# Kernel tuning notes

Measured on AMD Instinct MI355X. Metric: run time of the kernel, lower is better.

## Reference

```python
import jax, jax.numpy as jnp
import numpy as np

B = 1024; PAST = 64; FUT = 16; N = PAST + FUT; DM = N // 3; HID = 64
EMB = [(2000, 32), (7, 8), (24, 8)]
OUTP = 3 + 32 + 8 + 8  # 51 = out_preprocess
O = OUTP - 1           # 50
HID1 = 64; HID2 = 64
NEG = -1e30  # finite stand-in for -inf so fully-masked rows stay NaN-free


def _gcnn(x, A, W, act):
    # D = diag((1 + rowsum(sign(relu(A-1e-15))))^-0.5); out = act(D @ A @ D @ (x W^T))
    d = (1.0 + (A > 1e-15).astype(x.dtype).sum(1)) ** -0.5
    An = d[:, None] * A * d[None, :]            # (P,P)
    h = jnp.einsum('pq,bqc->bpc', An, x @ W.T)  # (B,P,out)
    return jax.nn.relu(h) if act else h


def _forward(data, emb0, emb1, emb2, w1, b1, w2, b2, w3, b3,
             M, Wg1a, Wg1b, Wk, smoothing, Wg2a, Wg2b):
    # learned adjacency: masked softmax over strictly-lower-triangular support
    mask = jnp.tril(jnp.ones((N, N), data.dtype), -1)
    A0 = jax.nn.relu(M @ M.T)
    A = jax.nn.softmax(jnp.where(mask > 0, A0, NEG), axis=1)
    A = jnp.where(mask > 0, A, 0.0)
    # pre_processing: embeddings + MLP, then re-append last raw column
    tabs = (emb0, emb1, emb2)
    e = [t[data[:, :, i].astype(jnp.int32)] for i, t in enumerate(tabs)]
    h = jnp.concatenate(e + [data[:, :, -3:]], -1)        # (B,N,51)
    h = jax.nn.relu(h @ w1.T + b1)
    h = jax.nn.relu(h @ w2.T + b2)
    h = h @ w3.T + b3                                      # (B,N,50)
    x = jnp.concatenate([h, data[:, :, -1:]], -1)          # (B,N,51)
    sg1, sg2 = x[:, :PAST], x[:, PAST:]
    A11 = A[:PAST, :PAST]
    x1 = _gcnn(_gcnn(sg1, A11, Wg1a, True), A11, Wg1b, False)   # (B,PAST,50)
    xk = jnp.concatenate([x1, sg2[:, :, :-1]], 1)               # (B,N,50)
    y = x[:, :PAST, -1:]                                        # (B,PAST,1)
    # Kernel: batched Mahalanobis quadratic form (diagonal computed directly)
    xp, xf = xk[:, :PAST], xk[:, PAST:]
    theta = Wk @ Wk.T
    theta = (theta + theta.T) / 2
    diff = xp[:, None, :, :] - xf[:, :, None, :]                # (B,F,P,50)
    q = jnp.einsum('bjip,pq,bjiq->bji', diff, theta, diff)      # (B,F,P)
    alpha = -0.5 * q / (jax.nn.sigmoid(smoothing[0]) * 0.01)
    At = A[FUT:, :PAST] if False else A[PAST:, :PAST]           # (F,P)
    At = jax.nn.softmax(jnp.where(At != 0, At, NEG), axis=1)
    # torch Softmax(dim=1) on (B,F,P) normalizes over the F axis
    alpha = jax.nn.softmax(jnp.where(At[None] >= 0.004, alpha, NEG), axis=1)
    yh = jnp.einsum('bjp,bpo->bjo', alpha, y)                   # (B,F,1)
    x2 = jnp.concatenate([sg2[:, :, :-1], yh], -1)              # (B,F,51)
    A22 = A[PAST:, PAST:]
    out = _gcnn(_gcnn(x2, A22, Wg2a, True), A22, Wg2b, False).reshape(-1, FUT)
    # cdist(x, x), p=2, with NaN-safe sqrt at zero distance
    xc = jnp.concatenate([sg1, x2], 1)                          # (B,N,51)
    sq = jnp.sum(xc * xc, -1)
    d2 = jnp.maximum(sq[:, :, None] + sq[:, None, :]
                     - 2.0 * jnp.einsum('bnc,bmc->bnm', xc, xc), 0.0)
    dist = jnp.where(d2 > 0, jnp.sqrt(jnp.where(d2 > 0, d2, 1.0)), 0.0)
    return (out, dist, A)


def setup_inputs() -> dict:
    key = jax.random.key(0)
    ks = jax.random.split(key, 20)
    cols = [jax.random.randint(ks[i], (B, N, 1), 0, EMB[i][0]).astype(jnp.float32)
            for i in range(3)]
    data = jnp.concatenate(cols + [jax.random.normal(ks[3], (B, N, 3), jnp.float32)], -1)
    g = lambda k, s, sc: jax.random.normal(k, s, jnp.float32) * sc
    return dict(
        data=data,
        emb0=g(ks[4], EMB[0], 1.0),
        emb1=g(ks[5], EMB[1], 1.0),
        emb2=g(ks[6], EMB[2], 1.0),
        w1=g(ks[7], (128, OUTP), OUTP ** -0.5), b1=jnp.zeros((128,), jnp.float32),
        w2=g(ks[8], (128, 128), 128 ** -0.5), b2=jnp.zeros((128,), jnp.float32),
        w3=g(ks[9], (O, 128), 128 ** -0.5), b3=jnp.zeros((O,), jnp.float32),
        M=g(ks[10], (N, DM), 1.0),
        Wg1a=g(ks[11], (HID1, OUTP), OUTP ** -0.5),
        Wg1b=g(ks[12], (O, HID1), HID1 ** -0.5),
        Wk=g(ks[13], (O, HID), 0.05),
        smoothing=g(ks[14], (1,), 1.0),
        Wg2a=g(ks[15], (HID2, OUTP), OUTP ** -0.5),
        Wg2b=g(ks[16], (1, HID2), HID2 ** -0.5),
    )


def reference(data, emb0, emb1, emb2, w1, b1, w2, b2, w3, b3,
              M, Wg1a, Wg1b, Wk, smoothing, Wg2a, Wg2b):
    return _forward(data, emb0, emb1, emb2, w1, b1, w2, b2, w3, b3,
                    M, Wg1a, Wg1b, Wk, smoothing, Wg2a, Wg2b)
```

## Files before the change

kernel.cpp:

```cpp
#include <hip/hip_runtime.h>
#include <math.h>


#define NEGBIG (-1e30f)

#define OFF_X     0
#define OFF_A     7471104
#define OFF_AN22  7481600
#define OFF_MK    7484356
#define OFF_GAH   7514692
#define OFF_GAL   7516740
#define OFF_G2AT  7521156
#define OFF_SC    7524420
#define OFF_W1H   7524424
#define OFF_W1L   7528520
#define OFF_W2H   7532616
#define OFF_W2L   7540808
#define OFF_W3H   7549000
#define OFF_W3L   7553096
#define OFF_ANH   7557192
#define OFF_ANL   7559240
#define OFF_GBH   7561288
#define OFF_GBL   7563336
#define OFF_WKH   7565384
#define OFF_WKL   7567432

#define OUT_OUT   0
#define OUT_DIST  16384
#define OUT_A     6569984

typedef __attribute__((ext_vector_type(8))) short bf16x8;
typedef __attribute__((ext_vector_type(4))) short s16x4;
typedef __attribute__((ext_vector_type(4))) float f32x4;

__device__ __forceinline__ unsigned short f2bf(float x) {
  union { float f; unsigned u; } v; v.f = x;
  unsigned r = v.u + 0x7fffu + ((v.u >> 16) & 1u);
  return (unsigned short)(r >> 16);
}
__device__ __forceinline__ float bf2f(unsigned short h) {
  union { unsigned u; float f; } v; v.u = ((unsigned)h) << 16; return v.f;
}
__device__ __forceinline__ void split2(float v, unsigned short& h, unsigned short& l) {
  unsigned short hh = f2bf(v);
  h = hh;
  l = f2bf(v - bf2f(hh));
}
#define SWZ6(r, k) (((r) << 6) + (((((k) >> 3) ^ ((r) & 7)) << 3) | ((k) & 7)))
#define SWZ7(r, k) (((r) << 7) + (((((k) >> 3) ^ ((r) & 7)) << 3) | ((k) & 7)))

#define MFMA3(acc, aH, aL, bH, bL) \
  acc = __builtin_amdgcn_mfma_f32_16x16x32_bf16(aH, bH, acc, 0, 0, 0); \
  acc = __builtin_amdgcn_mfma_f32_16x16x32_bf16(aH, bL, acc, 0, 0, 0); \
  acc = __builtin_amdgcn_mfma_f32_16x16x32_bf16(aL, bH, acc, 0, 0, 0);
#define MFMA4(acc, aH, aL, bH, bL) \
  MFMA3(acc, aH, aL, bH, bL) \
  acc = __builtin_amdgcn_mfma_f32_16x16x32_bf16(aL, bL, acc, 0, 0, 0);

__global__ __launch_bounds__(256) void k_prep(
    const float* __restrict__ M, const float* __restrict__ Wk,
    const float* __restrict__ sm,
    const float* __restrict__ w1, const float* __restrict__ w2,
    const float* __restrict__ w3,
    const float* __restrict__ wg1a, const float* __restrict__ wg1b,
    const float* __restrict__ wg2a,
    float* __restrict__ ws, float* __restrict__ out)
{
  __shared__ float Msh[80 * 26];
  __shared__ float Ash[80 * 80];
  __shared__ float d1[64];
  __shared__ float d2s[16];
  const int t = threadIdx.x;

  if (blockIdx.x == 0) {
    for (int e = t; e < 80 * 26; e += 256) Msh[e] = M[e];
    __syncthreads();
    for (int e = t; e < 6400; e += 256) {
      int i = e / 80, j = e % 80;
      float v = 0.f;
      if (j < i) {
        float s = 0.f;
        for (int k = 0; k < 26; ++k) s += Msh[i * 26 + k] * Msh[j * 26 + k];
        v = s > 0.f ? s : 0.f;
      }
      Ash[e] = v;
    }
    __syncthreads();
    if (t > 0 && t < 80) {
      int i = t;
      float m = -3.4e38f;
      for (int j = 0; j < i; ++j) m = fmaxf(m, Ash[i * 80 + j]);
      float s = 0.f;
      for (int j = 0; j < i; ++j) {
        float e = expf(Ash[i * 80 + j] - m);
        Ash[i * 80 + j] = e;
        s += e;
      }
      float inv = 1.f / s;
      for (int j = 0; j < i; ++j) Ash[i * 80 + j] *= inv;
    }
// ... 61 lines not shown
    }
    if (t == 0) {
      float v = sm[0];
      float sig = 1.f / (1.f + expf(-v));
      (ws + OFF_SC)[0] = -0.5f / (sig * 0.01f);
    }
  } else if (blockIdx.x == 2) {
    unsigned short* w1h = (unsigned short*)(ws + OFF_W1H);
    unsigned short* w1l = (unsigned short*)(ws + OFF_W1L);
    for (int e = t; e < 8192; e += 256) {
      int n = e >> 6, k = e & 63;
      float v = (k < 51) ? w1[n * 51 + k] : 0.f;
      unsigned short h = f2bf(v);
      w1h[e] = h; w1l[e] = f2bf(v - bf2f(h));
    }
    unsigned short* w3h = (unsigned short*)(ws + OFF_W3H);
    unsigned short* w3l = (unsigned short*)(ws + OFF_W3L);
    for (int e = t; e < 8192; e += 256) {
      int n = e >> 7, k = e & 127;
      float v = (n < 50) ? w3[n * 128 + k] : 0.f;
      unsigned short h = f2bf(v);
      w3h[e] = h; w3l[e] = f2bf(v - bf2f(h));
    }
    unsigned short* gah = (unsigned short*)(ws + OFF_GAH);
    unsigned short* gal = (unsigned short*)(ws + OFF_GAL);
    for (int e = t; e < 4096; e += 256) {
      int n = e >> 6, k = e & 63;
      float v = (k < 51) ? wg1a[n * 51 + k] : 0.f;
      unsigned short h = f2bf(v);
      gah[e] = h; gal[e] = f2bf(v - bf2f(h));
    }
  } else {
    unsigned short* w2h = (unsigned short*)(ws + OFF_W2H);
    unsigned short* w2l = (unsigned short*)(ws + OFF_W2L);
    for (int e = t; e < 16384; e += 256) {
      int n = e >> 7, k = e & 127;
      float v = w2[n * 128 + k];
      unsigned short h = f2bf(v);
      w2h[e] = h; w2l[e] = f2bf(v - bf2f(h));
    }
    unsigned short* gbh = (unsigned short*)(ws + OFF_GBH);
    unsigned short* gbl = (unsigned short*)(ws + OFF_GBL);
    for (int e = t; e < 4096; e += 256) {
      int n = e >> 6, k = e & 63;
      float v = (n < 50) ? wg1b[n * 64 + k] : 0.f;
      unsigned short h = f2bf(v);
      gbh[e] = h; gbl[e] = f2bf(v - bf2f(h));
    }
    float* g2at = ws + OFF_G2AT;
    for (int e = t; e < 64 * 51; e += 256) { int o = e / 51, k = e % 51; g2at[k * 64 + o] = wg2a[e]; }
  }
}

__global__ __launch_bounds__(512, 4) void k_fused(
    const float* __restrict__ data,
    const float* __restrict__ emb0, const float* __restrict__ emb1,
    const float* __restrict__ emb2,
    const float* __restrict__ b1v, const float* __restrict__ b2v,
    const float* __restrict__ b3v,
    const float* __restrict__ wg2b,
    float* __restrict__ ws, float* __restrict__ out)
{
  __shared__ __align__(16) unsigned short SH[32768];
  __shared__ __align__(16) float xbuf[80 * 51];

  const int t = threadIdx.x, b = blockIdx.x;
  const int lane = t & 63, wave = t >> 6;
  const int m16 = lane & 15, quad = lane >> 4;

  {
    unsigned short* mIaH = SH;
    unsigned short* mIaL = SH + 5120;
    unsigned short* mHdH = SH + 10240;
    unsigned short* mHdL = SH + 20480;
    const unsigned short* w1h = (const unsigned short*)(ws + OFF_W1H);
    const unsigned short* w1l = (const unsigned short*)(ws + OFF_W1L);
    const unsigned short* w2h = (const unsigned short*)(ws + OFF_W2H);
    const unsigned short* w2l = (const unsigned short*)(ws + OFF_W2L);
    const unsigned short* w3h = (const unsigned short*)(ws + OFF_W3H);
    const unsigned short* w3l = (const unsigned short*)(ws + OFF_W3L);

    for (int e = t; e < 5120; e += 512) {
      int r = e >> 6, c = e & 63;
      int g = b * 80 + r;
      float v = 0.f;
      if (c < 32)      { int i0 = (int)data[g * 6 + 0]; v = emb0[i0 * 32 + c]; }
      else if (c < 40) { int i1 = (int)data[g * 6 + 1]; v = emb1[i1 * 8 + (c - 32)]; }
      else if (c < 48) { int i2 = (int)data[g * 6 + 2]; v = emb2[i2 * 8 + (c - 40)]; }
      else if (c < 51) { v = data[g * 6 + 3 + (c - 48)]; }
      int idx = SWZ6(r, c);
      split2(v, mIaH[idx], mIaL[idx]);
    }
    if (t < 80) xbuf[t * 51 + 50] = data[(b * 80 + t) * 6 + 5];
    __syncthreads();

    {
      const int col = wave * 16 + m16;
      bf16x8 bH0 = *(const bf16x8*)(w1h + (col << 6) + (quad << 3));
      bf16x8 bL0 = *(const bf16x8*)(w1l + (col << 6) + (quad << 3));
      bf16x8 bH1 = *(const bf16x8*)(w1h + (col << 6) + ((quad + 4) << 3));
      bf16x8 bL1 = *(const bf16x8*)(w1l + (col << 6) + ((quad + 4) << 3));
      const float bias = b1v[col];
      const int ach0 = ((quad + 0) ^ (m16 & 7)) << 3;
      const int ach1 = ((quad + 4) ^ (m16 & 7)) << 3;
#pragma unroll
      for (int rt = 0; rt < 5; ++rt) {
        const int ar = rt * 16 + m16;
        f32x4 acc = (f32x4){0.f, 0.f, 0.f, 0.f};
        bf16x8 aH = *(const bf16x8*)(mIaH + (ar << 6) + ach0);
        bf16x8 aL = *(const bf16x8*)(mIaL + (ar << 6) + ach0);
        MFMA3(acc, aH, aL, bH0, bL0)
        aH = *(const bf16x8*)(mIaH + (ar << 6) + ach1);
        aL = *(const bf16x8*)(mIaL + (ar << 6) + ach1);
        MFMA3(acc, aH, aL, bH1, bL1)
#pragma unroll
        for (int r = 0; r < 4; ++r) {
          float v = acc[r] + bias; v = v > 0.f ? v : 0.f;
          int idx = SWZ7(rt * 16 + quad * 4 + r, col);
          split2(v, mHdH[idx], mHdL[idx]);
        }
      }
    }
    __syncthreads();

    f32x4 acc2[5];
    {
      const int col = wave * 16 + m16;
      bf16x8 bh[4], bl[4];
#pragma unroll
      for (int kk = 0; kk < 4; ++kk) {
        bh[kk] = *(const bf16x8*)(w2h + (col << 7) + ((quad + kk * 4) << 3));
        bl[kk] = *(const bf16x8*)(w2l + (col << 7) + ((quad + kk * 4) << 3));
      }
#pragma unroll
      for (int rt = 0; rt < 5; ++rt) {
        const int ar = rt * 16 + m16;
        f32x4 acc = (f32x4){0.f, 0.f, 0.f, 0.f};
#pragma unroll
        for (int kk = 0; kk < 4; ++kk) {
          int ach = ((quad + kk * 4) ^ (m16 & 7)) << 3;
          bf16x8 aH = *(const bf16x8*)(mHdH + (ar << 7) + ach);
          bf16x8 aL = *(const bf16x8*)(mHdL + (ar << 7) + ach);
          MFMA3(acc, aH, aL, bh[kk], bl[kk])
        }
        acc2[rt] = acc;
      }
    }
    __syncthreads();
    {
      const int col = wave * 16 + m16;
      const float bias = b2v[col];
#pragma unroll
      for (int rt = 0; rt < 5; ++rt) {
#pragma unroll
        for (int r = 0; r < 4; ++r) {
          float v = acc2[rt][r] + bias; v = v > 0.f ? v : 0.f;
          int idx = SWZ7(rt * 16 + quad * 4 + r, col);
          split2(v, mHdH[idx], mHdL[idx]);
        }
      }
    }
    __syncthreads();

    {
      const int ct = wave & 3, rh = wave >> 2;
      const int col = ct * 16 + m16;
      bf16x8 bh[4], bl[4];
#pragma unroll
      for (int kk = 0; kk < 4; ++kk) {
        bh[kk] = *(const bf16x8*)(w3h + (col << 7) + ((quad + kk * 4) << 3));
        bl[kk] = *(const bf16x8*)(w3l + (col << 7) + ((quad + kk * 4) << 3));
      }
      const float bias = (col < 50) ? b3v[col] : 0.f;
      for (int rt = rh; rt < 5; rt += 2) {
        const int ar = rt * 16 + m16;
        f32x4 acc = (f32x4){0.f, 0.f, 0.f, 0.f};
#pragma unroll
        for (int kk = 0; kk < 4; ++kk) {
          int ach = ((quad + kk * 4) ^ (m16 & 7)) << 3;
          bf16x8 aH = *(const bf16x8*)(mHdH + (ar << 7) + ach);
          bf16x8 aL = *(const bf16x8*)(mHdL + (ar << 7) + ach);
          MFMA3(acc, aH, aL, bh[kk], bl[kk])
        }
        if (col < 50) {
#pragma unroll
          for (int r = 0; r < 4; ++r)
            xbuf[(rt * 16 + quad * 4 + r) * 51 + col] = acc[r] + bias;
        }
      }
    }
    __syncthreads();
  }

  unsigned short* b1H = SH;
  unsigned short* b1L = SH + 4096;
  unsigned short* b2H = SH + 8192;
  unsigned short* b2L = SH + 12288;
  unsigned short* anH = SH + 16384;
  unsigned short* anL = SH + 20480;
  unsigned short* wH  = SH + 24576;
  unsigned short* wL  = SH + 28672;
  unsigned short* xfH = SH + 24576;
  unsigned short* xfL = SH + 25600;
  unsigned short* zfH = SH + 26624;
  unsigned short* zfL = SH + 27648;
  float* alS  = (float*)(SH + 28672);
  float* spH2 = (float*)(SH + 30848);
  float* spS  = (float*)(SH + 31104);
  float* sfS  = (float*)(SH + 31232);
  float* yvS  = (float*)(SH + 31264);
  float* yhsS = (float*)(SH + 31392);
  float* X2v  = (float*)(SH + 8192);
  float* A22v = X2v + 832;
  float* G2v  = A22v + 256;
  float* Pmv  = G2v + 1024;
  float* wb2  = Pmv + 1024;
  float* zzv  = wb2 + 64;
  unsigned short* xcH = SH;
  unsigned short* xcL = SH + 16384;
  float* sqS = (float*)(SH + 21504);

  const int s = wave & 3, half = wave >> 2;
  const int row0 = s * 16;
  const int arow = row0 + m16;
  const float* mk = ws + OFF_MK;
  const float* an22 = ws + OFF_AN22;
  const float* g2at = ws + OFF_G2AT;
  const unsigned short* gAnH = (const unsigned short*)(ws + OFF_ANH);
  const unsigned short* gAnL = (const unsigned short*)(ws + OFF_ANL);
  const unsigned short* gaH = (const unsigned short*)(ws + OFF_GAH);
  const unsigned short* gaL = (const unsigned short*)(ws + OFF_GAL);
  const unsigned short* gbH = (const unsigned short*)(ws + OFF_GBH);
  const unsigned short* gbL = (const unsigned short*)(ws + OFF_GBL);
  const unsigned short* gwkH = (const unsigned short*)(ws + OFF_WKH);
  const unsigned short* gwkL = (const unsigned short*)(ws + OFF_WKL);
  const float sc = (ws + OFF_SC)[0];

  for (int e = t; e < 4096; e += 512) {
    int r = e >> 6, k = e & 63;
    float v = (k < 51) ? xbuf[r * 51 + k] : 0.f;
    int idx = SWZ6(r, k);
    split2(v, b1H[idx], b1L[idx]);
  }
  {
    int q = t;
    if (q < 512) {
      int r = q >> 3, c = q & 7;
      int dst = (r << 6) + ((c ^ (r & 7)) << 3);
      int src = (r << 6) + (c << 3);
      *(bf16x8*)(anH + dst) = *(const bf16x8*)(gAnH + src);
      *(bf16x8*)(anL + dst) = *(const bf16x8*)(gAnL + src);
      *(bf16x8*)(wH + dst)  = *(const bf16x8*)(gaH + src);
      *(bf16x8*)(wL + dst)  = *(const bf16x8*)(gaL + src);
    }
  }
  float yvreg = 0.f;
  if (t < 64) yvreg = xbuf[t * 51 + 50];
  bf16x8 pH, pL;
  {
    int q = t & 511;
    int r = q >> 3, c = q & 7;
    int src = (r << 6) + (c << 3);
    pH = *(const bf16x8*)(gbH + src);
    pL = *(const bf16x8*)(gbL + src);
  }
  __syncthreads();

  f32x4 accA[2];
#pragma unroll
  for (int n = 0; n < 2; ++n) accA[n] = (f32x4){0.f, 0.f, 0.f, 0.f};
#pragma unroll
  for (int kb8 = 0; kb8 < 8; kb8 += 4) {
    int ach = ((quad + kb8) ^ (m16 & 7)) << 3;
    bf16x8 aH = *(const bf16x8*)(b1H + (arow << 6) + ach);
    bf16x8 aL = *(const bf16x8*)(b1L + (arow << 6) + ach);
#pragma unroll
    for (int n = 0; n < 2; ++n) {
      const int col = (half * 2 + n) * 16 + m16;
      int boff = (col << 6) + ach;
      bf16x8 bH = *(const bf16x8*)(wH + boff);
      bf16x8 bL = *(const bf16x8*)(wL + boff);
      MFMA3(accA[n], aH, aL, bH, bL)
    }
  }
  __syncthreads();

  {
    const int kb = row0 + quad * 4;
#pragma unroll
    for (int n = 0; n < 2; ++n) {
      const int col = (half * 2 + n) * 16 + m16;
      int idx = (col << 6) + (((((kb >> 3) ^ (col & 7)) << 3)) | (kb & 7));
      s16x4 hv, lv;
#pragma unroll
      for (int r = 0; r < 4; ++r) {
        unsigned short hh, ll; split2(accA[n][r], hh, ll);
        hv[r] = (short)hh; lv[r] = (short)ll;
      }
      *(s16x4*)(b2H + idx) = hv; *(s16x4*)(b2L + idx) = lv;
    }
  }
  {
    int q = t & 511;
    int r = q >> 3, c = q & 7;
    int dst = (r << 6) + ((c ^ (r & 7)) << 3);
    *(bf16x8*)(wH + dst) = pH;
    *(bf16x8*)(wL + dst) = pL;
    int src = (r << 6) + (c << 3);
    pH = *(const bf16x8*)(gwkH + src);
    pL = *(const bf16x8*)(gwkL + src);
  }
  __syncthreads();

#pragma unroll
  for (int n = 0; n < 2; ++n) accA[n] = (f32x4){0.f, 0.f, 0.f, 0.f};
#pragma unroll
  for (int kb8 = 0; kb8 < 8; kb8 += 4) {
    int ach = ((quad + kb8) ^ (m16 & 7)) << 3;
    bf16x8 aH = *(const bf16x8*)(anH + (arow << 6) + ach);
    bf16x8 aL = *(const bf16x8*)(anL + (arow << 6) + ach);
#pragma unroll
    for (int n = 0; n < 2; ++n) {
      const int col = (half * 2 + n) * 16 + m16;
      int boff = (col << 6) + ach;
      bf16x8 bH = *(const bf16x8*)(b2H + boff);
      bf16x8 bL = *(const bf16x8*)(b2L + boff);
      MFMA3(accA[n], aH, aL, bH, bL)
    }
  }
  __syncthreads();

  {
    const int kb = row0 + quad * 4;
#pragma unroll
    for (int n = 0; n < 2; ++n) {
      const int col = (half * 2 + n) * 16 + m16;
      int idx = (col << 6) + (((((kb >> 3) ^ (col & 7)) << 3)) | (kb & 7));
      s16x4 hv, lv;
#pragma unroll
      for (int r = 0; r < 4; ++r) {
        float v = accA[n][r]; v = v > 0.f ? v : 0.f;
        unsigned short hh, ll; split2(v, hh, ll);
        hv[r] = (short)hh; lv[r] = (short)ll;
      }
      *(s16x4*)(b2H + idx) = hv; *(s16x4*)(b2L + idx) = lv;
    }
  }
  __syncthreads();

#pragma unroll
  for (int n = 0; n < 2; ++n) accA[n] = (f32x4){0.f, 0.f, 0.f, 0.f};
#pragma unroll
  for (int kb8 = 0; kb8 < 8; kb8 += 4) {
    int ach = ((quad + kb8) ^ (m16 & 7)) << 3;
    bf16x8 aH = *(const bf16x8*)(anH + (arow << 6) + ach);
    bf16x8 aL = *(const bf16x8*)(anL + (arow << 6) + ach);
#pragma unroll
    for (int n = 0; n < 2; ++n) {
      const int col = (half * 2 + n) * 16 + m16;
      int boff = (col << 6) + ach;
      bf16x8 bH = *(const bf16x8*)(b2H + boff);
      bf16x8 bL = *(const bf16x8*)(b2L + boff);
      MFMA3(accA[n], aH, aL, bH, bL)
    }
  }
  __syncthreads();

#pragma unroll
  for (int n = 0; n < 2; ++n) {
    const int col = (half * 2 + n) * 16 + m16;
#pragma unroll
    for (int r = 0; r < 4; ++r) {
      int idx = SWZ6(row0 + quad * 4 + r, col);
      split2(accA[n][r], b1H[idx], b1L[idx]);
    }
  }
  {
    int q = t & 511;
    int r = q >> 3, c = q & 7;
    int dst = (r << 6) + ((c ^ (r & 7)) << 3);
    *(bf16x8*)(anH + dst) = pH;
    *(bf16x8*)(anL + dst) = pL;
  }
  float xf0 = 0.f, xf1 = 0.f;
  {
    int e0 = t, e1 = t + 512;
    int r0r = e0 >> 6, c0 = e0 & 63;
    int r1r = e1 >> 6, c1 = e1 & 63;
    if (c0 < 50) xf0 = xbuf[(64 + r0r) * 51 + c0];
    if (c1 < 50) xf1 = xbuf[(64 + r1r) * 51 + c1];
  }
  __syncthreads();

#pragma unroll
  for (int n = 0; n < 2; ++n) accA[n] = (f32x4){0.f, 0.f, 0.f, 0.f};
#pragma unroll
  for (int kb8 = 0; kb8 < 8; kb8 += 4) {
    int ach = ((quad + kb8) ^ (m16 & 7)) << 3;
    bf16x8 aH = *(const bf16x8*)(b1H + (arow << 6) + ach);
    bf16x8 aL = *(const bf16x8*)(b1L + (arow << 6) + ach);
#pragma unroll
    for (int n = 0; n < 2; ++n) {
      const int col = (half * 2 + n) * 16 + m16;
      int boff = (col << 6) + ach;
      bf16x8 bH = *(const bf16x8*)(wH + boff);
      bf16x8 bL = *(const bf16x8*)(wL + boff);
      MFMA3(accA[n], aH, aL, bH, bL)
    }
  }
  __syncthreads();

#pragma unroll
  for (int n = 0; n < 2; ++n) {
    const int col = (half * 2 + n) * 16 + m16;
#pragma unroll
    for (int r = 0; r < 4; ++r) {
      int idx = SWZ6(row0 + quad * 4 + r, col);
      split2(accA[n][r], b2H[idx], b2L[idx]);
    }
  }
  {
    int e0 = t, e1 = t + 512;
    int i0 = SWZ6(e0 >> 6, e0 & 63);
    int i1 = SWZ6(e1 >> 6, e1 & 63);
    split2(xf0, xfH[i0], xfL[i0]);
    split2(xf1, xfH[i1], xfL[i1]);
  }
  if (t < 64) yvS[t] = yvreg;
  __syncthreads();

#pragma unroll
  for (int n = 0; n < 2; ++n) accA[n] = (f32x4){0.f, 0.f, 0.f, 0.f};
#pragma unroll
  for (int kb8 = 0; kb8 < 8; kb8 += 4) {
    int ach = ((quad + kb8) ^ (m16 & 7)) << 3;
    bf16x8 aH = *(const bf16x8*)(b2H + (arow << 6) + ach);
    bf16x8 aL = *(const bf16x8*)(b2L + (arow << 6) + ach);
#pragma unroll
    for (int n = 0; n < 2; ++n) {
      const int col = (half * 2 + n) * 16 + m16;
      int boff = (col << 6) + ach;
      bf16x8 bH = *(const bf16x8*)(anH + boff);
      bf16x8 bL = *(const bf16x8*)(anL + boff);
      MFMA4(accA[n], aH, aL, bH, bL)
    }
  }
  if (half == 0) {
    f32x4 af = (f32x4){0.f, 0.f, 0.f, 0.f};
#pragma unroll
    for (int kb8 = 0; kb8 < 8; kb8 += 4) {
      int ach = ((quad + kb8) ^ (m16 & 7)) << 3;
      bf16x8 aH = *(const bf16x8*)(xfH + (m16 << 6) + ach);
      bf16x8 aL = *(const bf16x8*)(xfL + (m16 << 6) + ach);
      const int col = s * 16 + m16;
      int boff = (col << 6) + ach;
      bf16x8 bH = *(const bf16x8*)(anH + boff);
      bf16x8 bL = *(const bf16x8*)(anL + boff);
      MFMA4(af, aH, aL, bH, bL)
    }
    const int h = s * 16 + m16;
#pragma unroll
    for (int r = 0; r < 4; ++r) {
      int idx = SWZ6(quad * 4 + r, h);
      split2(af[r], zfH[idx], zfL[idx]);
    }
  }
  {
    float s2[4];
#pragma unroll
    for (int r = 0; r < 4; ++r)
      s2[r] = accA[0][r] * accA[0][r] + accA[1][r] * accA[1][r];
#pragma unroll
    for (int n = 0; n < 2; ++n) {
      const int h = (half * 2 + n) * 16 + m16;
#pragma unroll
      for (int r = 0; r < 4; ++r) {
        int idx = SWZ6(row0 + quad * 4 + r, h);
        split2(accA[n][r], b1H[idx], b1L[idx]);
      }
    }
#pragma unroll
    for (int m = 1; m < 16; m <<= 1)
#pragma unroll
      for (int r = 0; r < 4; ++r) s2[r] += __shfl_xor(s2[r], m);
    if (m16 == 0) {
#pragma unroll
      for (int r = 0; r < 4; ++r)
        spH2[(row0 + quad * 4 + r) * 2 + half] = s2[r];
    }
  }
  __syncthreads();

  if (t < 64) {
    spS[t] = spH2[t * 2] + spH2[t * 2 + 1];
  } else if (t < 320) {
    int idx = t - 64;
    int j = idx >> 4, h0 = (idx & 15) * 4;
    float p = 0.f;
#pragma unroll
    for (int r = 0; r < 4; ++r) {
      int ii = SWZ6(j, h0 + r);
      float v = bf2f(zfH[ii]) + bf2f(zfL[ii]);
      p += v * v;
    }
#pragma unroll
    for (int m = 1; m < 16; m <<= 1) p += __shfl_xor(p, m);
    if ((idx & 15) == 0) sfS[j] = p;
  }
  __syncthreads();

  {
    f32x4 ac2 = (f32x4){0.f, 0.f, 0.f, 0.f};
#pragma unroll
    for (int kb8 = 0; kb8 < 8; kb8 += 4) {
      int ach = ((quad + kb8) ^ (m16 & 7)) << 3;
      bf16x8 aH = *(const bf16x8*)(b1H + (arow << 6) + ach);
      bf16x8 aL = *(const bf16x8*)(b1L + (arow << 6) + ach);
      bf16x8 bH = *(const bf16x8*)(zfH + (m16 << 6) + ach);
      bf16x8 bL = *(const bf16x8*)(zfL + (m16 << 6) + ach);
      MFMA4(ac2, aH, aL, bH, bL)
    }
    if (half == 0) {
#pragma unroll
      for (int r = 0; r < 4; ++r) {
        int i = row0 + quad * 4 + r;
        alS[i * 17 + m16] = sc * (spS[i] + sfS[m16] - 2.f * ac2[r]);
      }
    }
  }
  __syncthreads();

  if (t < 64) {
    const int i = t;
    float lv[16];
    float m = -3.4e38f;
#pragma unroll
    for (int j = 0; j < 16; ++j) {
      float v = (mk[j * 64 + i] != 0.f) ? alS[i * 17 + j] : NEGBIG;
      lv[j] = v;
      m = fmaxf(m, v);
    }
    float ssum = 0.f;
#pragma unroll
    for (int j = 0; j < 16; ++j) { lv[j] = expf(lv[j] - m); ssum += lv[j]; }
    float inv = 1.f / ssum;
#pragma unroll
    for (int j = 0; j < 16; ++j) alS[i * 17 + j] = lv[j] * inv;
  }
  __syncthreads();

  if (t < 256) {
    int j = t >> 4, i0 = (t & 15) * 4;
    float p = 0.f;
#pragma unroll
    for (int r = 0; r < 4; ++r) p += alS[(i0 + r) * 17 + j] * yvS[i0 + r];
#pragma unroll
    for (int m = 1; m < 16; m <<= 1) p += __shfl_xor(p, m);
    if ((t & 15) == 0) yhsS[j] = p;
  }
  __syncthreads();

  for (int e = t; e < 5120; e += 512) {
    int n = e >> 6, c = e & 63;
    float v = 0.f;
    if (c < 50)       v = xbuf[n * 51 + c];
    else if (c == 50) v = (n < 64) ? xbuf[n * 51 + 50] : yhsS[n - 64];
    int idx = SWZ6(n, c);
    split2(v, xcH[idx], xcL[idx]);
  }
  for (int e = t; e < 832; e += 512) {
    int r = e / 52, c = e - r * 52;
    float v = 0.f;
    if (c < 50)       v = xbuf[(64 + r) * 51 + c];
    else if (c == 50) v = yhsS[r];
    X2v[e] = v;
  }
  for (int e = t; e < 256; e += 512) A22v[e] = an22[e];
  if (t < 64) wb2[t] = wg2b[t];
  __syncthreads();

  f32x4 accD[4];
  {
    int tc = 0;
    for (int idx = wave; idx < 25; idx += 8) {
      int ts = idx / 5, tf = idx - ts * 5;
      f32x4 acc = (f32x4){0.f, 0.f, 0.f, 0.f};
#pragma unroll
      for (int kb8 = 0; kb8 < 8; kb8 += 4) {
        int ach = ((quad + kb8) ^ (m16 & 7)) << 3;
        bf16x8 aH = *(const bf16x8*)(xcH + ((ts * 16 + m16) << 6) + ach);
        bf16x8 aL = *(const bf16x8*)(xcL + ((ts * 16 + m16) << 6) + ach);
        const int col = tf * 16 + m16;
        int boff = (col << 6) + ach;
        bf16x8 bH = *(const bf16x8*)(xcH + boff);
        bf16x8 bL = *(const bf16x8*)(xcL + boff);
        MFMA3(acc, aH, aL, bH, bL)
      }
      if (ts == tf && (m16 >> 2) == quad) sqS[ts * 16 + m16] = acc[m16 & 3];
      accD[tc++] = acc;
    }
  }
  for (int e = t; e < 1024; e += 512) {
    int j = e >> 6, h = e & 63;
    float ssum = 0.f;
    for (int k = 0; k < 51; ++k) ssum += X2v[j * 52 + k] * g2at[k * 64 + h];
    G2v[e] = ssum;
  }
  __syncthreads();

  for (int e = t; e < 1024; e += 512) {
    int j = e >> 6, h = e & 63;
    float ssum = 0.f;
#pragma unroll
    for (int k = 0; k < 16; ++k) ssum += A22v[j * 16 + k] * G2v[k * 64 + h];
    Pmv[e] = ssum > 0.f ? ssum : 0.f;
  }
  {
    float* dist = out + OUT_DIST + b * 6400;
    int tc = 0;
    for (int idx = wave; idx < 25; idx += 8) {
      int ts = idx / 5, tf = idx - ts * 5;
      f32x4 acc = accD[tc++];
#pragma unroll
      for (int r = 0; r < 4; ++r) {
        int i = ts * 16 + quad * 4 + r;
        int m = tf * 16 + m16;
        float d2 = sqS[i] + sqS[m] - 2.f * acc[r];
        d2 = d2 > 0.f ? d2 : 0.f;
        dist[i * 80 + m] = d2 > 0.f ? sqrtf(d2) : 0.f;
      }
    }
  }
  __syncthreads();
  if (t < 256) {
    int j = t >> 4, h0 = (t & 15) * 4;
    float p = 0.f;
#pragma unroll
    for (int r = 0; r < 4; ++r) p += Pmv[j * 64 + h0 + r] * wb2[h0 + r];
#pragma unroll
    for (int m = 1; m < 16; m <<= 1) p += __shfl_xor(p, m);
    if ((t & 15) == 0) zzv[j] = p;
  }
  __syncthreads();
  if (t < 16) {
    float ssum = 0.f;
#pragma unroll
    for (int k = 0; k < 16; ++k) ssum += A22v[t * 16 + k] * zzv[k];
    out[OUT_OUT + b * 16 + t] = ssum;
  }
}

extern "C" void kernel_launch(void* const* d_in, const int* in_sizes, int n_in,
                              void* d_out, int out_size, void* d_ws, size_t ws_size,
                              hipStream_t stream)
{
  const float* data = (const float*)d_in[0];
  const float* emb0 = (const float*)d_in[1];
  const float* emb1 = (const float*)d_in[2];
  const float* emb2 = (const float*)d_in[3];
  const float* w1   = (const float*)d_in[4];
  const float* b1   = (const float*)d_in[5];
  const float* w2   = (const float*)d_in[6];
  const float* b2   = (const float*)d_in[7];
  const float* w3   = (const float*)d_in[8];
  const float* b3   = (const float*)d_in[9];
  const float* M    = (const float*)d_in[10];
  const float* wg1a = (const float*)d_in[11];
  const float* wg1b = (const float*)d_in[12];
  const float* Wk   = (const float*)d_in[13];
  const float* smo  = (const float*)d_in[14];
  const float* wg2a = (const float*)d_in[15];
  const float* wg2b = (const float*)d_in[16];
  float* ws  = (float*)d_ws;
  float* out = (float*)d_out;

  k_prep <<<dim3(4),    dim3(256), 0, stream>>>(M, Wk, smo, w1, w2, w3, wg1a, wg1b, wg2a, ws, out);
  k_fused<<<dim3(1024), dim3(512), 0, stream>>>(data, emb0, emb1, emb2, b1, b2, b3, wg2b, ws, out);
}
```

Baseline: 200.3 us.

## Shrink shared memory footprint to raise occupancy and stream weights from global

The MLP preprocessing now runs over rows in two chunks (48 then 32) so hidden activations need less LDS, and embeddings are gathered straight into MFMA A-fragments in registers instead of staging through shared memory. The fp32 xbuf is dropped and the features are kept only as split bf16 in xc. The GCNN and kernel weight operands are read directly from global memory instead of being copied into LDS, which removes several barriers. LDS drops from about 80KB to 54KB and launch bounds rise to 6 blocks per SM, trading extra global/L2 traffic and recomputed bf16 reconstructions for higher occupancy.

```diff
diff --git a/kernel.cpp b/kernel.cpp
--- a/kernel.cpp
+++ b/kernel.cpp
@@ -4,7 +4,6 @@
 
 #define NEGBIG (-1e30f)
 
-#define OFF_X     0
 #define OFF_A     7471104
 #define OFF_AN22  7481600
 #define OFF_MK    7484356
@@ -46,6 +45,13 @@
   h = hh;
   l = f2bf(v - bf2f(hh));
 }
+__device__ __forceinline__ void split8(const float* v, bf16x8& h8, bf16x8& l8) {
+#pragma unroll
+  for (int j = 0; j < 8; ++j) {
+    unsigned short hh, ll; split2(v[j], hh, ll);
+    h8[j] = (short)hh; l8[j] = (short)ll;
+  }
+}
 #define SWZ6(r, k) (((r) << 6) + (((((k) >> 3) ^ ((r) & 7)) << 3) | ((k) & 7)))
 #define SWZ7(r, k) (((r) << 7) + (((((k) >> 3) ^ ((r) & 7)) << 3) | ((k) & 7)))
 
@@ -213,7 +219,7 @@
   }
 }
 
-__global__ __launch_bounds__(512, 4) void k_fused(
+__global__ __launch_bounds__(512, 6) void k_fused(
     const float* __restrict__ data,
     const float* __restrict__ emb0, const float* __restrict__ emb1,
     const float* __restrict__ emb2,
@@ -222,168 +228,44 @@
     const float* __restrict__ wg2b,
     float* __restrict__ ws, float* __restrict__ out)
 {
-  __shared__ __align__(16) unsigned short SH[32768];
-  __shared__ __align__(16) float xbuf[80 * 51];
+  __shared__ __align__(16) unsigned short SH[27136];
+
+  unsigned short* xcH = SH;
+  unsigned short* xcL = SH + 5120;
+  unsigned short* b1H = SH + 10240;
+  unsigned short* b1L = SH + 14336;
+  unsigned short* b2H = SH + 18432;
+  unsigned short* b2L = SH + 22528;
+  float* spH2 = (float*)(SH + 26624);
+  float* spS  = (float*)(SH + 26880);
+  float* sfS  = (float*)(SH + 27008);
+  float* yhsS = (float*)(SH + 27040);
+  float* alS = (float*)(SH + 18432);
+  unsigned short* zfH = SH + 22528;
+  unsigned short* zfL = SH + 23552;
+  unsigned short* mHdH = SH + 10240;
+  unsigned short* mHdL = SH + 16384;
+  float* X2v  = (float*)(SH + 10240);
+  float* A22v = (float*)(SH + 11904);
+  float* G2v  = (float*)(SH + 12416);
+  float* Pmv  = (float*)(SH + 14464);
+  float* wb2  = (float*)(SH + 16512);
+  float* zzv  = (float*)(SH + 16640);
+  float* sqS  = (float*)(SH + 16672);
 
   const int t = threadIdx.x, b = blockIdx.x;
   const int lane = t & 63, wave = t >> 6;
   const int m16 = lane & 15, quad = lane >> 4;
-
-  {
-    unsigned short* mIaH = SH;
-    unsigned short* mIaL = SH + 5120;
-    unsigned short* mHdH = SH + 10240;
-    unsigned short* mHdL = SH + 20480;
-    const unsigned short* w1h = (const unsigned short*)(ws + OFF_W1H);
-    const unsigned short* w1l = (const unsigned short*)(ws + OFF_W1L);
-    const unsigned short* w2h = (const unsigned short*)(ws + OFF_W2H);
-    const unsigned short* w2l = (const unsigned short*)(ws + OFF_W2L);
-    const unsigned short* w3h = (const unsigned short*)(ws + OFF_W3H);
-    const unsigned short* w3l = (const unsigned short*)(ws + OFF_W3L);
-
-    for (int e = t; e < 5120; e += 512) {
-      int r = e >> 6, c = e & 63;
-      int g = b * 80 + r;
-      float v = 0.f;
-      if (c < 32)      { int i0 = (int)data[g * 6 + 0]; v = emb0[i0 * 32 + c]; }
-      else if (c < 40) { int i1 = (int)data[g * 6 + 1]; v = emb1[i1 * 8 + (c - 32)]; }
-      else if (c < 48) { int i2 = (int)data[g * 6 + 2]; v = emb2[i2 * 8 + (c - 40)]; }
-      else if (c < 51) { v = data[g * 6 + 3 + (c - 48)]; }
-      int idx = SWZ6(r, c);
-      split2(v, mIaH[idx], mIaL[idx]);
-    }
-    if (t < 80) xbuf[t * 51 + 50] = data[(b * 80 + t) * 6 + 5];
-    __syncthreads();
-
-    {
-      const int col = wave * 16 + m16;
-      bf16x8 bH0 = *(const bf16x8*)(w1h + (col << 6) + (quad << 3));
-      bf16x8 bL0 = *(const bf16x8*)(w1l + (col << 6) + (quad << 3));
-      bf16x8 bH1 = *(const bf16x8*)(w1h + (col << 6) + ((quad + 4) << 3));
-      bf16x8 bL1 = *(const bf16x8*)(w1l + (col << 6) + ((quad + 4) << 3));
-      const float bias = b1v[col];
-      const int ach0 = ((quad + 0) ^ (m16 & 7)) << 3;
-      const int ach1 = ((quad + 4) ^ (m16 & 7)) << 3;
-#pragma unroll
-      for (int rt = 0; rt < 5; ++rt) {
-        const int ar = rt * 16 + m16;
-        f32x4 acc = (f32x4){0.f, 0.f, 0.f, 0.f};
-        bf16x8 aH = *(const bf16x8*)(mIaH + (ar << 6) + ach0);
-        bf16x8 aL = *(const bf16x8*)(mIaL + (ar << 6) + ach0);
-        MFMA3(acc, aH, aL, bH0, bL0)
-        aH = *(const bf16x8*)(mIaH + (ar << 6) + ach1);
-        aL = *(const bf16x8*)(mIaL + (ar << 6) + ach1);
-        MFMA3(acc, aH, aL, bH1, bL1)
-#pragma unroll
-        for (int r = 0; r < 4; ++r) {
-          float v = acc[r] + bias; v = v > 0.f ? v : 0.f;
-          int idx = SWZ7(rt * 16 + quad * 4 + r, col);
-          split2(v, mHdH[idx], mHdL[idx]);
-        }
-      }
-    }
-    __syncthreads();
-
-    f32x4 acc2[5];
-    {
-      const int col = wave * 16 + m16;
-      bf16x8 bh[4], bl[4];
-#pragma unroll
-      for (int kk = 0; kk < 4; ++kk) {
-        bh[kk] = *(const bf16x8*)(w2h + (col << 7) + ((quad + kk * 4) << 3));
-        bl[kk] = *(const bf16x8*)(w2l + (col << 7) + ((quad + kk * 4) << 3));
-      }
-#pragma unroll
-      for (int rt = 0; rt < 5; ++rt) {
-        const int ar = rt * 16 + m16;
-        f32x4 acc = (f32x4){0.f, 0.f, 0.f, 0.f};
-#pragma unroll
-        for (int kk = 0; kk < 4; ++kk) {
-          int ach = ((quad + kk * 4) ^ (m16 & 7)) << 3;
-          bf16x8 aH = *(const bf16x8*)(mHdH + (ar << 7) + ach);
-          bf16x8 aL = *(const bf16x8*)(mHdL + (ar << 7) + ach);
-          MFMA3(acc, aH, aL, bh[kk], bl[kk])
-        }
-        acc2[rt] = acc;
-      }
-    }
-    __syncthreads();
-    {
-      const int col = wave * 16 + m16;
-      const float bias = b2v[col];
-#pragma unroll
-      for (int rt = 0; rt < 5; ++rt) {
-#pragma unroll
-        for (int r = 0; r < 4; ++r) {
-          float v = acc2[rt][r] + bias; v = v > 0.f ? v : 0.f;
-          int idx = SWZ7(rt * 16 + quad * 4 + r, col);
-          split2(v, mHdH[idx], mHdL[idx]);
-        }
-      }
-    }
-    __syncthreads();
-
-    {
-      const int ct = wave & 3, rh = wave >> 2;
-      const int col = ct * 16 + m16;
-      bf16x8 bh[4], bl[4];
-#pragma unroll
-      for (int kk = 0; kk < 4; ++kk) {
-        bh[kk] = *(const bf16x8*)(w3h + (col << 7) + ((quad + kk * 4) << 3));
-        bl[kk] = *(const bf16x8*)(w3l + (col << 7) + ((quad + kk * 4) << 3));
-      }
-      const float bias = (col < 50) ? b3v[col] : 0.f;
-      for (int rt = rh; rt < 5; rt += 2) {
-        const int ar = rt * 16 + m16;
-        f32x4 acc = (f32x4){0.f, 0.f, 0.f, 0.f};
-#pragma unroll
-        for (int kk = 0; kk < 4; ++kk) {
-          int ach = ((quad + kk * 4) ^ (m16 & 7)) << 3;
-          bf16x8 aH = *(const bf16x8*)(mHdH + (ar << 7) + ach);
-          bf16x8 aL = *(const bf16x8*)(mHdL + (ar << 7) + ach);
-          MFMA3(acc, aH, aL, bh[kk], bl[kk])
-        }
-        if (col < 50) {
-#pragma unroll
-          for (int r = 0; r < 4; ++r)
-            xbuf[(rt * 16 + quad * 4 + r) * 51 + col] = acc[r] + bias;
-        }
-      }
-    }
-    __syncthreads();
-  }
-
-  unsigned short* b1H = SH;
-  unsigned short* b1L = SH + 4096;
-  unsigned short* b2H = SH + 8192;
-  unsigned short* b2L = SH + 12288;
-  unsigned short* anH = SH + 16384;
-  unsigned short* anL = SH + 20480;
-  unsigned short* wH  = SH + 24576;
-  unsigned short* wL  = SH + 28672;
-  unsigned short* xfH = SH + 24576;
-  unsigned short* xfL = SH + 25600;
-  unsigned short* zfH = SH + 26624;
-  unsigned short* zfL = SH + 27648;
-  float* alS  = (float*)(SH + 28672);
-  float* spH2 = (float*)(SH + 30848);
-  float* spS  = (float*)(SH + 31104);
-  float* sfS  = (float*)(SH + 31232);
-  float* yvS  = (float*)(SH + 31264);
-  float* yhsS = (float*)(SH + 31392);
-  float* X2v  = (float*)(SH + 8192);
-  float* A22v = X2v + 832;
-  float* G2v  = A22v + 256;
-  float* Pmv  = G2v + 1024;
-  float* wb2  = Pmv + 1024;
-  float* zzv  = wb2 + 64;
-  unsigned short* xcH = SH;
-  unsigned short* xcL = SH + 16384;
-  float* sqS = (float*)(SH + 21504);
-
   const int s = wave & 3, half = wave >> 2;
   const int row0 = s * 16;
   const int arow = row0 + m16;
+
+  const unsigned short* w1h = (const unsigned short*)(ws + OFF_W1H);
+  const unsigned short* w1l = (const unsigned short*)(ws + OFF_W1L);
+  const unsigned short* w2h = (const unsigned short*)(ws + OFF_W2H);
+  const unsigned short* w2l = (const unsigned short*)(ws + OFF_W2L);
+  const unsigned short* w3h = (const unsigned short*)(ws + OFF_W3H);
+  const unsigned short* w3l = (const unsigned short*)(ws + OFF_W3L);
   const float* mk = ws + OFF_MK;
   const float* an22 = ws + OFF_AN22;
   const float* g2at = ws + OFF_G2AT;
@@ -397,55 +279,156 @@
   const unsigned short* gwkL = (const unsigned short*)(ws + OFF_WKL);
   const float sc = (ws + OFF_SC)[0];
 
-  for (int e = t; e < 4096; e += 512) {
-    int r = e >> 6, k = e & 63;
-    float v = (k < 51) ? xbuf[r * 51 + k] : 0.f;
-    int idx = SWZ6(r, k);
-    split2(v, b1H[idx], b1L[idx]);
-  }
-  {
-    int q = t;
-    if (q < 512) {
-      int r = q >> 3, c = q & 7;
-      int dst = (r << 6) + ((c ^ (r & 7)) << 3);
-      int src = (r << 6) + (c << 3);
-      *(bf16x8*)(anH + dst) = *(const bf16x8*)(gAnH + src);
-      *(bf16x8*)(anL + dst) = *(const bf16x8*)(gAnL + src);
-      *(bf16x8*)(wH + dst)  = *(const bf16x8*)(gaH + src);
-      *(bf16x8*)(wL + dst)  = *(const bf16x8*)(gaL + src);
-    }
-  }
-  float yvreg = 0.f;
-  if (t < 64) yvreg = xbuf[t * 51 + 50];
-  bf16x8 pH, pL;
-  {
-    int q = t & 511;
-    int r = q >> 3, c = q & 7;
-    int src = (r << 6) + (c << 3);
-    pH = *(const bf16x8*)(gbH + src);
-    pL = *(const bf16x8*)(gbL + src);
-  }
-  __syncthreads();
+#pragma unroll
+  for (int ck = 0; ck < 2; ++ck) {
+    const int C0 = ck ? 48 : 0;
+    const int NT = ck ? 2 : 3;
+
+    {
+      const int col = wave * 16 + m16;
+      bf16x8 bH0 = *(const bf16x8*)(w1h + (col << 6) + (quad << 3));
+      bf16x8 bL0 = *(const bf16x8*)(w1l + (col << 6) + (quad << 3));
+      bf16x8 bH1 = *(const bf16x8*)(w1h + (col << 6) + 32 + (quad << 3));
+      bf16x8 bL1 = *(const bf16x8*)(w1l + (col << 6) + 32 + (quad << 3));
+      const float bias = b1v[col];
+#pragma unroll
+      for (int rt = 0; rt < NT; ++rt) {
+        const int g = b * 80 + C0 + rt * 16 + m16;
+        float v0[8], v1[8];
+        {
+          int i0 = (int)data[g * 6 + 0];
+          const float* p = emb0 + i0 * 32 + (quad << 3);
+#pragma unroll
+          for (int j = 0; j < 8; ++j) v0[j] = p[j];
+        }
+        if (quad == 0) {
+          int i1 = (int)data[g * 6 + 1];
+#pragma unroll
+          for (int j = 0; j < 8; ++j) v1[j] = emb1[i1 * 8 + j];
+        } else if (quad == 1) {
+          int i2 = (int)data[g * 6 + 2];
+#pragma unroll
+          for (int j = 0; j < 8; ++j) v1[j] = emb2[i2 * 8 + j];
+        } else if (quad == 2) {
+          v1[0] = data[g * 6 + 3]; v1[1] = data[g * 6 + 4]; v1[2] = data[g * 6 + 5];
+#pragma unroll
+          for (int j = 3; j < 8; ++j) v1[j] = 0.f;
+        } else {
+#pragma unroll
+          for (int j = 0; j < 8; ++j) v1[j] = 0.f;
+        }
+        bf16x8 aH0, aL0, aH1, aL1;
+        split8(v0, aH0, aL0);
+        split8(v1, aH1, aL1);
+        f32x4 acc = (f32x4){0.f, 0.f, 0.f, 0.f};
+        MFMA3(acc, aH0, aL0, bH0, bL0)
+        MFMA3(acc, aH1, aL1, bH1, bL1)
+#pragma unroll
+        for (int r = 0; r < 4; ++r) {
+          float v = acc[r] + bias; v = v > 0.f ? v : 0.f;
+          int idx = SWZ7(rt * 16 + quad * 4 + r, col);
+          split2(v, mHdH[idx], mHdL[idx]);
+        }
+      }
+    }
+    __syncthreads();
+
+    f32x4 acc2[3];
+    {
+      const int col = wave * 16 + m16;
+      bf16x8 bh[4], bl[4];
+#pragma unroll
+      for (int kk = 0; kk < 4; ++kk) {
+        bh[kk] = *(const bf16x8*)(w2h + (col << 7) + ((quad + kk * 4) << 3));
+        bl[kk] = *(const bf16x8*)(w2l + (col << 7) + ((quad + kk * 4) << 3));
+      }
+#pragma unroll
+      for (int lrt = 0; lrt < NT; ++lrt) {
+        const int lr = lrt * 16 + m16;
+        f32x4 acc = (f32x4){0.f, 0.f, 0.f, 0.f};
+#pragma unroll
+        for (int kk = 0; kk < 4; ++kk) {
+          int ach = ((quad + kk * 4) ^ (m16 & 7)) << 3;
+          bf16x8 aH = *(const bf16x8*)(mHdH + (lr << 7) + ach);
+          bf16x8 aL = *(const bf16x8*)(mHdL + (lr << 7) + ach);
+          MFMA3(acc, aH, aL, bh[kk], bl[kk])
+        }
+        acc2[lrt] = acc;
+      }
+    }
+    __syncthreads();
+
+    {
+      const int col = wave * 16 + m16;
+      const float bias = b2v[col];
+#pragma unroll
+      for (int lrt = 0; lrt < NT; ++lrt) {
+#pragma unroll
+        for (int r = 0; r < 4; ++r) {
+          float v = acc2[lrt][r] + bias; v = v > 0.f ? v : 0.f;
+          int idx = SWZ7(lrt * 16 + quad * 4 + r, col);
+          split2(v, mHdH[idx], mHdL[idx]);
+        }
+      }
+    }
+    __syncthreads();
+
+    {
+      const int colt = wave & 3, rh = wave >> 2;
+      const int col = colt * 16 + m16;
+      bf16x8 bh[4], bl[4];
+#pragma unroll
+      for (int kk = 0; kk < 4; ++kk) {
+        bh[kk] = *(const bf16x8*)(w3h + (col << 7) + ((quad + kk * 4) << 3));
+        bl[kk] = *(const bf16x8*)(w3l + (col << 7) + ((quad + kk * 4) << 3));
+      }
+      const float bias = (col < 50) ? b3v[col] : 0.f;
+      for (int lrt = rh; lrt < NT; lrt += 2) {
+        const int lr = lrt * 16 + m16;
+        f32x4 acc = (f32x4){0.f, 0.f, 0.f, 0.f};
+#pragma unroll
+        for (int kk = 0; kk < 4; ++kk) {
+          int ach = ((quad + kk * 4) ^ (m16 & 7)) << 3;
+          bf16x8 aH = *(const bf16x8*)(mHdH + (lr << 7) + ach);
+          bf16x8 aL = *(const bf16x8*)(mHdL + (lr << 7) + ach);
+          MFMA3(acc, aH, aL, bh[kk], bl[kk])
+        }
+        if (col != 50) {
+#pragma unroll
+          for (int r = 0; r < 4; ++r) {
+            int grow = C0 + lrt * 16 + quad * 4 + r;
+            int idx = SWZ6(grow, col);
+            split2(acc[r] + bias, xcH[idx], xcL[idx]);
+          }
+        }
+      }
+      if (ck == 0 && t < 80) {
+        float v = (t < 64) ? data[(b * 80 + t) * 6 + 5] : 0.f;
+        int idx = SWZ6(t, 50);
+        split2(v, xcH[idx], xcL[idx]);
+      }
+    }
+    __syncthreads();
+  }
 
   f32x4 accA[2];
+
 #pragma unroll
   for (int n = 0; n < 2; ++n) accA[n] = (f32x4){0.f, 0.f, 0.f, 0.f};
 #pragma unroll
   for (int kb8 = 0; kb8 < 8; kb8 += 4) {
     int ach = ((quad + kb8) ^ (m16 & 7)) << 3;
-    bf16x8 aH = *(const bf16x8*)(b1H + (arow << 6) + ach);
-    bf16x8 aL = *(const bf16x8*)(b1L + (arow << 6) + ach);
+    int k0 = (quad + kb8) << 3;
+    bf16x8 aH = *(const bf16x8*)(xcH + (arow << 6) + ach);
+    bf16x8 aL = *(const bf16x8*)(xcL + (arow << 6) + ach);
 #pragma unroll
     for (int n = 0; n < 2; ++n) {
       const int col = (half * 2 + n) * 16 + m16;
-      int boff = (col << 6) + ach;
-      bf16x8 bH = *(const bf16x8*)(wH + boff);
-      bf16x8 bL = *(const bf16x8*)(wL + boff);
+      bf16x8 bH = *(const bf16x8*)(gaH + (col << 6) + k0);
+      bf16x8 bL = *(const bf16x8*)(gaL + (col << 6) + k0);
       MFMA3(accA[n], aH, aL, bH, bL)
     }
   }
-  __syncthreads();
-
   {
     const int kb = row0 + quad * 4;
 #pragma unroll
@@ -461,16 +444,6 @@
       *(s16x4*)(b2H + idx) = hv; *(s16x4*)(b2L + idx) = lv;
     }
   }
-  {
-    int q = t & 511;
-    int r = q >> 3, c = q & 7;
-    int dst = (r << 6) + ((c ^ (r & 7)) << 3);
-    *(bf16x8*)(wH + dst) = pH;
-    *(bf16x8*)(wL + dst) = pL;
-    int src = (r << 6) + (c << 3);
-    pH = *(const bf16x8*)(gwkH + src);
-    pL = *(const bf16x8*)(gwkL + src);
-  }
   __syncthreads();
 
 #pragma unroll
@@ -478,8 +451,9 @@
 #pragma unroll
   for (int kb8 = 0; kb8 < 8; kb8 += 4) {
     int ach = ((quad + kb8) ^ (m16 & 7)) << 3;
-    bf16x8 aH = *(const bf16x8*)(anH + (arow << 6) + ach);
-    bf16x8 aL = *(const bf16x8*)(anL + (arow << 6) + ach);
+    int k0 = (quad + kb8) << 3;
+    bf16x8 aH = *(const bf16x8*)(gAnH + (arow << 6) + k0);
+    bf16x8 aL = *(const bf16x8*)(gAnL + (arow << 6) + k0);
 #pragma unroll
     for (int n = 0; n < 2; ++n) {
       const int col = (half * 2 + n) * 16 + m16;
@@ -514,8 +488,9 @@
 #pragma unroll
   for (int kb8 = 0; kb8 < 8; kb8 += 4) {
     int ach = ((quad + kb8) ^ (m16 & 7)) << 3;
-    bf16x8 aH = *(const bf16x8*)(anH + (arow << 6) + ach);
-    bf16x8 aL = *(const bf16x8*)(anL + (arow << 6) + ach);
+    int k0 = (quad + kb8) << 3;
+    bf16x8 aH = *(const bf16x8*)(gAnH + (arow << 6) + k0);
+    bf16x8 aL = *(const bf16x8*)(gAnL + (arow << 6) + k0);
 #pragma unroll
     for (int n = 0; n < 2; ++n) {
       const int col = (half * 2 + n) * 16 + m16;
@@ -525,8 +500,6 @@
       MFMA3(accA[n], aH, aL, bH, bL)
     }
   }
-  __syncthreads();
-
 #pragma unroll
   for (int n = 0; n < 2; ++n) {
     const int col = (half * 2 + n) * 16 + m16;
@@ -536,21 +509,6 @@
       split2(accA[n][r], b1H[idx], b1L[idx]);
     }
   }
-  {
-    int q = t & 511;
-    int r = q >> 3, c = q & 7;
-    int dst = (r << 6) + ((c ^ (r & 7)) << 3);
-    *(bf16x8*)(anH + dst) = pH;
-    *(bf16x8*)(anL + dst) = pL;
-  }
-  float xf0 = 0.f, xf1 = 0.f;
-  {
-    int e0 = t, e1 = t + 512;
-    int r0r = e0 >> 6, c0 = e0 & 63;
-    int r1r = e1 >> 6, c1 = e1 & 63;
-    if (c0 < 50) xf0 = xbuf[(64 + r0r) * 51 + c0];
-    if (c1 < 50) xf1 = xbuf[(64 + r1r) * 51 + c1];
-  }
   __syncthreads();
 
 #pragma unroll
@@ -558,19 +516,17 @@
 #pragma unroll
   for (int kb8 = 0; kb8 < 8; kb8 += 4) {
     int ach = ((quad + kb8) ^ (m16 & 7)) << 3;
+    int k0 = (quad + kb8) << 3;
     bf16x8 aH = *(const bf16x8*)(b1H + (arow << 6) + ach);
     bf16x8 aL = *(const bf16x8*)(b1L + (arow << 6) + ach);
 #pragma unroll
     for (int n = 0; n < 2; ++n) {
       const int col = (half * 2 + n) * 16 + m16;
-      int boff = (col << 6) + ach;
-      bf16x8 bH = *(const bf16x8*)(wH + boff);
-      bf16x8 bL = *(const bf16x8*)(wL + boff);
+      bf16x8 bH = *(const bf16x8*)(gbH + (col << 6) + k0);
+      bf16x8 bL = *(const bf16x8*)(gbL + (col << 6) + k0);
       MFMA3(accA[n], aH, aL, bH, bL)
     }
   }
-  __syncthreads();
-
 #pragma unroll
   for (int n = 0; n < 2; ++n) {
     const int col = (half * 2 + n) * 16 + m16;
@@ -580,45 +536,66 @@
       split2(accA[n][r], b2H[idx], b2L[idx]);
     }
   }
-  {
-    int e0 = t, e1 = t + 512;
-    int i0 = SWZ6(e0 >> 6, e0 & 63);
-    int i1 = SWZ6(e1 >> 6, e1 & 63);
-    split2(xf0, xfH[i0], xfL[i0]);
-    split2(xf1, xfH[i1], xfL[i1]);
-  }
-  if (t < 64) yvS[t] = yvreg;
   __syncthreads();
 
 #pragma unroll
   for (int n = 0; n < 2; ++n) accA[n] = (f32x4){0.f, 0.f, 0.f, 0.f};
+  f32x4 af = (f32x4){0.f, 0.f, 0.f, 0.f};
 #pragma unroll
   for (int kb8 = 0; kb8 < 8; kb8 += 4) {
     int ach = ((quad + kb8) ^ (m16 & 7)) << 3;
+    int k0 = (quad + kb8) << 3;
     bf16x8 aH = *(const bf16x8*)(b2H + (arow << 6) + ach);
     bf16x8 aL = *(const bf16x8*)(b2L + (arow << 6) + ach);
 #pragma unroll
     for (int n = 0; n < 2; ++n) {
       const int col = (half * 2 + n) * 16 + m16;
-      int boff = (col << 6) + ach;
-      bf16x8 bH = *(const bf16x8*)(anH + boff);
-      bf16x8 bL = *(const bf16x8*)(anL + boff);
+      bf16x8 bH = *(const bf16x8*)(gwkH + (col << 6) + k0);
+      bf16x8 bL = *(const bf16x8*)(gwkL + (col << 6) + k0);
       MFMA4(accA[n], aH, aL, bH, bL)
     }
   }
   if (half == 0) {
-    f32x4 af = (f32x4){0.f, 0.f, 0.f, 0.f};
 #pragma unroll
     for (int kb8 = 0; kb8 < 8; kb8 += 4) {
       int ach = ((quad + kb8) ^ (m16 & 7)) << 3;
-      bf16x8 aH = *(const bf16x8*)(xfH + (m16 << 6) + ach);
-      bf16x8 aL = *(const bf16x8*)(xfL + (m16 << 6) + ach);
+      int k0 = (quad + kb8) << 3;
+      bf16x8 aH = *(const bf16x8*)(xcH + ((64 + m16) << 6) + ach);
+      bf16x8 aL = *(const bf16x8*)(xcL + ((64 + m16) << 6) + ach);
       const int col = s * 16 + m16;
-      int boff = (col << 6) + ach;
-      bf16x8 bH = *(const bf16x8*)(anH + boff);
-      bf16x8 bL = *(const bf16x8*)(anL + boff);
+      bf16x8 bH = *(const bf16x8*)(gwkH + (col << 6) + k0);
+      bf16x8 bL = *(const bf16x8*)(gwkL + (col << 6) + k0);
       MFMA4(af, aH, aL, bH, bL)
     }
+  }
+  {
+    float s2[4];
+#pragma unroll
+    for (int r = 0; r < 4; ++r)
+      s2[r] = accA[0][r] * accA[0][r] + accA[1][r] * accA[1][r];
+#pragma unroll
+    for (int n = 0; n < 2; ++n) {
+      const int h = (half * 2 + n) * 16 + m16;
+#pragma unroll
+      for (int r = 0; r < 4; ++r) {
+        int idx = SWZ6(row0 + quad * 4 + r, h);
+        split2(accA[n][r], b1H[idx], b1L[idx]);
+      }
+    }
+#pragma unroll
+    for (int m = 1; m < 16; m <<= 1)
+#pragma unroll
+      for (int r = 0; r < 4; ++r) s2[r] += __shfl_xor(s2[r], m);
+    if (m16 == 0) {
+#pragma unroll
+      for (int r = 0; r < 4; ++r)
+        spH2[(row0 + quad * 4 + r) * 2 + half] = s2[r];
+    }
+  }
+  __syncthreads();
+
+  if (t < 64) spS[t] = spH2[t * 2] + spH2[t * 2 + 1];
+  if (half == 0) {
     const int h = s * 16 + m16;
 #pragma unroll
     for (int r = 0; r < 4; ++r) {
@@ -626,52 +603,10 @@
       split2(af[r], zfH[idx], zfL[idx]);
     }
   }
-  {
-    float s2[4];
-#pragma unroll
-    for (int r = 0; r < 4; ++r)
-      s2[r] = accA[0][r] * accA[0][r] + accA[1][r] * accA[1][r];
-#pragma unroll
-    for (int n = 0; n < 2; ++n) {
-      const int h = (half * 2 + n) * 16 + m16;
-#pragma unroll
-      for (int r = 0; r < 4; ++r) {
-        int idx = SWZ6(row0 + quad * 4 + r, h);
-        split2(accA[n][r], b1H[idx], b1L[idx]);
-      }
-    }
-#pragma unroll
-    for (int m = 1; m < 16; m <<= 1)
-#pragma unroll
-      for (int r = 0; r < 4; ++r) s2[r] += __shfl_xor(s2[r], m);
-    if (m16 == 0) {
-#pragma unroll
-      for (int r = 0; r < 4; ++r)
-        spH2[(row0 + quad * 4 + r) * 2 + half] = s2[r];
-    }
-  }
-  __syncthreads();
-
-  if (t < 64) {
-    spS[t] = spH2[t * 2] + spH2[t * 2 + 1];
-  } else if (t < 320) {
-    int idx = t - 64;
-    int j = idx >> 4, h0 = (idx & 15) * 4;
-    float p = 0.f;
-#pragma unroll
-    for (int r = 0; r < 4; ++r) {
-      int ii = SWZ6(j, h0 + r);
-      float v = bf2f(zfH[ii]) + bf2f(zfL[ii]);
-      p += v * v;
-    }
-#pragma unroll
-    for (int m = 1; m < 16; m <<= 1) p += __shfl_xor(p, m);
-    if ((idx & 15) == 0) sfS[j] = p;
-  }
-  __syncthreads();
-
-  {
-    f32x4 ac2 = (f32x4){0.f, 0.f, 0.f, 0.f};
+  __syncthreads();
+
+  f32x4 ac2 = (f32x4){0.f, 0.f, 0.f, 0.f};
+  if (half == 0) {
 #pragma unroll
     for (int kb8 = 0; kb8 < 8; kb8 += 4) {
       int ach = ((quad + kb8) ^ (m16 & 7)) << 3;
@@ -681,12 +616,27 @@
       bf16x8 bL = *(const bf16x8*)(zfL + (m16 << 6) + ach);
       MFMA4(ac2, aH, aL, bH, bL)
     }
-    if (half == 0) {
-#pragma unroll
-      for (int r = 0; r < 4; ++r) {
-        int i = row0 + quad * 4 + r;
-        alS[i * 17 + m16] = sc * (spS[i] + sfS[m16] - 2.f * ac2[r]);
-      }
+  } else {
+    int idx = t - 256;
+    int j = idx >> 4, h0 = (idx & 15) << 2;
+    float p = 0.f;
+#pragma unroll
+    for (int r = 0; r < 4; ++r) {
+      int ii = SWZ6(j, h0 + r);
+      float v = bf2f(zfH[ii]) + bf2f(zfL[ii]);
+      p += v * v;
+    }
+#pragma unroll
+    for (int m = 1; m < 16; m <<= 1) p += __shfl_xor(p, m);
+    if ((idx & 15) == 0) sfS[j] = p;
+  }
+  __syncthreads();
+
+  if (half == 0) {
+#pragma unroll
+    for (int r = 0; r < 4; ++r) {
+      int i = row0 + quad * 4 + r;
+      alS[i * 17 + m16] = sc * (spS[i] + sfS[m16] - 2.f * ac2[r]);
     }
   }
   __syncthreads();
@@ -711,29 +661,32 @@
   __syncthreads();
 
   if (t < 256) {
-    int j = t >> 4, i0 = (t & 15) * 4;
+    int j = t >> 4, i0 = (t & 15) << 2;
     float p = 0.f;
 #pragma unroll
-    for (int r = 0; r < 4; ++r) p += alS[(i0 + r) * 17 + j] * yvS[i0 + r];
+    for (int r = 0; r < 4; ++r) {
+      int i = i0 + r;
+      int iy = SWZ6(i, 50);
+      float yv = bf2f(xcH[iy]) + bf2f(xcL[iy]);
+      p += alS[i * 17 + j] * yv;
+    }
 #pragma unroll
     for (int m = 1; m < 16; m <<= 1) p += __shfl_xor(p, m);
     if ((t & 15) == 0) yhsS[j] = p;
   }
   __syncthreads();
 
-  for (int e = t; e < 5120; e += 512) {
-    int n = e >> 6, c = e & 63;
-    float v = 0.f;
-    if (c < 50)       v = xbuf[n * 51 + c];
-    else if (c == 50) v = (n < 64) ? xbuf[n * 51 + 50] : yhsS[n - 64];
-    int idx = SWZ6(n, c);
-    split2(v, xcH[idx], xcL[idx]);
+  if (t < 16) {
+    int idx = SWZ6(64 + t, 50);
+    split2(yhsS[t], xcH[idx], xcL[idx]);
   }
   for (int e = t; e < 832; e += 512) {
     int r = e / 52, c = e - r * 52;
     float v = 0.f;
-    if (c < 50)       v = xbuf[(64 + r) * 51 + c];
-    else if (c == 50) v = yhsS[r];
+    if (c < 50) {
+      int i6 = SWZ6(64 + r, c);
+      v = bf2f(xcH[i6]) + bf2f(xcL[i6]);
+    } else if (c == 50) v = yhsS[r];
     X2v[e] = v;
   }
   for (int e = t; e < 256; e += 512) A22v[e] = an22[e];
@@ -794,7 +747,7 @@
   }
   __syncthreads();
   if (t < 256) {
-    int j = t >> 4, h0 = (t & 15) * 4;
+    int j = t >> 4, h0 = (t & 15) << 2;
     float p = 0.f;
 #pragma unroll
     for (int r = 0; r < 4; ++r) p += Pmv[j * 64 + h0 + r] * wb2[h0 + r];
```

Result: slower. 258.2 us (+28.9%).
